# Optimization experiments

Hardware: AMD Instinct MI355X
Metric: run time of the kernel (lower is better)

## Reference

```python
import jax, jax.numpy as jnp
import numpy as np

D_MODEL = 1024
N_HEADS = 16
D_K = D_MODEL // N_HEADS
THETA = 10000.0


def _rope(x, token_positions):
    # x: [b, h, s, d_k]; interleaved RoPE (pairs at even/odd positions)
    half = D_K // 2
    inv_freq = 1.0 / (THETA ** (2.0 * jnp.arange(half, dtype=jnp.float32) / D_K))  # [half]
    angles = token_positions.astype(jnp.float32)[:, None] * inv_freq[None, :]      # [s, half]
    sin, cos = jnp.sin(angles), jnp.cos(angles)
    x_even = x[..., 0::2]
    x_odd = x[..., 1::2]
    out_even = cos * x_even - sin * x_odd
    out_odd = sin * x_even + cos * x_odd
    # interleave back: [..., half, 2] -> [..., d_k]
    return jnp.stack((out_even, out_odd), axis=-1).reshape(x.shape)


def setup_inputs() -> dict:
    key = jax.random.key(0)
    kx, kq, kk, kv, ko = jax.random.split(key, 5)
    b, s = 4, 2048
    std = (2.0 / (D_MODEL + D_MODEL)) ** 0.5
    return {
        "x": jax.random.normal(kx, (b, s, D_MODEL), dtype=jnp.float32),
        "Wq": jax.random.normal(kq, (D_MODEL, D_MODEL), dtype=jnp.float32) * std,
        "Wk": jax.random.normal(kk, (D_MODEL, D_MODEL), dtype=jnp.float32) * std,
        "Wv": jax.random.normal(kv, (D_MODEL, D_MODEL), dtype=jnp.float32) * std,
        "Wo": jax.random.normal(ko, (D_MODEL, D_MODEL), dtype=jnp.float32) * std,
        "token_positions": jnp.arange(s, dtype=jnp.int32),
    }


def reference(x, Wq, Wk, Wv, Wo, token_positions):
    b, s, _ = x.shape
    split = lambda t: t.reshape(b, s, N_HEADS, D_K).transpose(0, 2, 1, 3)  # b h s d
    q = split(x @ Wq.T)
    k = split(x @ Wk.T)
    v = split(x @ Wv.T)
    q = _rope(q, token_positions)
    k = _rope(k, token_positions)
    scores = jnp.einsum("bhnd,bhmd->bhnm", q, k) / jnp.sqrt(jnp.float32(D_K))
    causal = jnp.tril(jnp.ones((s, s), dtype=bool))
    scores = jnp.where(causal, scores, -jnp.inf)
    attn = jax.nn.softmax(scores, axis=-1)
    out = jnp.einsum("bhnm,bhmd->bhnd", attn, v)
    out = out.transpose(0, 2, 1, 3).reshape(b, s, D_MODEL)
    return out @ Wo.T
```

## Files before the change

kernel.cpp:

```cpp
#include <hip/hip_runtime.h>
#include <stdint.h>

typedef __attribute__((ext_vector_type(8))) __bf16 bf16x8;
typedef __attribute__((ext_vector_type(4))) float f32x4;
typedef __attribute__((ext_vector_type(16))) float f32x16;
typedef __attribute__((ext_vector_type(8))) unsigned short ushort8;

__device__ __forceinline__ unsigned short f2bf(float f){
  union { float f; unsigned int i; } v; v.f = f;
  unsigned int r = v.i + 0x7fffu + ((v.i >> 16) & 1u);
  return (unsigned short)(r >> 16);
}
__device__ __forceinline__ void gload16(const void* g, void* l){
  __builtin_amdgcn_global_load_lds((__attribute__((address_space(1))) void*)(g),
                                   (__attribute__((address_space(3))) void*)(l),
                                   16, 0, 0);
}
__device__ __forceinline__ unsigned int cvtpk(float lo, float hi){
  unsigned int r;
  asm("v_cvt_pk_bf16_f32 %0, %1, %2" : "=v"(r) : "v"(lo), "v"(hi));
  return r;
}
__device__ __forceinline__ float fexp2(float x){
  float r; asm("v_exp_f32 %0, %1" : "=v"(r) : "v"(x)); return r;
}
__device__ __forceinline__ bf16x8 ldsw(const char* tile, int row, int colb){
  return *(const bf16x8*)(tile + row*128 + (colb ^ ((row & 7) << 4)));
}

#define SEQ   2048
#define DM    1024
#define NH    16
#define DK    64
#define BATCH 4
#define MTOT  (BATCH*SEQ)
#define NX    (MTOT*DM)
#define NW    (DM*DM)

#define QSCALE 0.18033688011112f

__global__ __launch_bounds__(256) void k_tables(const int* __restrict__ pos,
                                                float* __restrict__ tab)
{
  const int idx = blockIdx.x * 256 + threadIdx.x;
  const int s = idx >> 5, i = idx & 31;
  const float inv = __expf(-0.28782313662425575f * (float)i);
  const float a = (float)pos[s] * inv;
  tab[2*idx]   = cosf(a);
  tab[2*idx+1] = sinf(a);
}

__global__ __launch_bounds__(256) void k_convert(
    const float* __restrict__ x,  const float* __restrict__ wq,
    const float* __restrict__ wk, const float* __restrict__ wv,
    const float* __restrict__ wo,
    unsigned short* __restrict__ xb, unsigned short* __restrict__ wb)
{
  const int tid = blockIdx.x * 256 + threadIdx.x;
  const long long e = (long long)tid * 8;
  const float* src; unsigned short* dst;
  if (e < NX) { src = x + e; dst = xb + e; }
  else {
    long long j = e - NX;
    int seg = (int)(j >> 20);
    long long off = j & 1048575;
    src = (seg==0?wq:seg==1?wk:seg==2?wv:wo) + off;
    dst = wb + (size_t)seg*NW + off;
  }
  const float4 a = *(const float4*)src;
  const float4 b = *(const float4*)(src + 4);
  uint4 o;
  o.x = (unsigned int)f2bf(a.x) | ((unsigned int)f2bf(a.y) << 16);
  o.y = (unsigned int)f2bf(a.z) | ((unsigned int)f2bf(a.w) << 16);
  o.z = (unsigned int)f2bf(b.x) | ((unsigned int)f2bf(b.y) << 16);
  o.w = (unsigned int)f2bf(b.z) | ((unsigned int)f2bf(b.w) << 16);
  *(uint4*)dst = o;
}

#define NT32 32
#define ABUF32  16384
#define BSTR32  24576

template<int MODE>
__global__ __launch_bounds__(512, 4) void k_gemm(
    const unsigned short* __restrict__ A,
    const unsigned short* __restrict__ Wb,
    unsigned short* __restrict__ D0,
    unsigned short* __restrict__ D1,
    unsigned short* __restrict__ D2,
    float* __restrict__ Dout,
    const float* __restrict__ tab)
{
  __shared__ __attribute__((aligned(16))) char lds_[3*BSTR32];
  const int tid  = threadIdx.x;
  const int lane = tid & 63;
  const int w    = tid >> 6;
  const int wm = w >> 1, wn = w & 1;

  const int bid = blockIdx.x;
  const int tq  = bid >> 3;
  const int m0  = ((bid & 7)*4 + (tq & 3)) * 256;
  const int r   = tq >> 2;
  const int n0  = (MODE == 0 ? (r & 7) : r) * 128;
  const int z   = (MODE == 0) ? (r >> 3) : 0;

  const unsigned short* W = Wb + (size_t)z * NW;
  unsigned short* Dh = (MODE == 0) ? ((z == 0) ? D0 : (z == 1) ? D1 : D2) : nullptr;
  const bool vtr = (MODE == 0) && (z == 2);

  f32x4 acc[4][4];
  #pragma unroll
  for (int i = 0; i < 4; ++i)
    #pragma unroll
    for (int j = 0; j < 4; ++j)
      acc[i][j] = (f32x4)0.0f;

  auto stA = [&](int buf, int t, int l){
    const int id = l*512 + tid;
    const int row = id >> 2, c = id & 3;
    gload16(A + (size_t)(m0 + row)*DM + t*32 + ((c ^ ((row >> 1) & 3)) << 3),
            lds_ + buf*BSTR32 + id*16);
  };
  auto stB = [&](int buf, int t){
    const int id = tid;
    const int row = id >> 2, c = id & 3;
    gload16(W + (size_t)(n0 + row)*DM + t*32 + ((c ^ ((row >> 1) & 3)) << 3),
            lds_ + buf*BSTR32 + ABUF32 + id*16);
  };
  auto ldA = [&](const char* Ab_, int i){
    const int row = wm*64 + i*16 + (lane & 15);
    const int c = (lane >> 4) ^ ((row >> 1) & 3);
    return *(const bf16x8*)(Ab_ + row*64 + (c << 4));
  };
  auto ldB = [&](const char* Bb_, int j){
    const int row = wn*64 + j*16 + (lane & 15);
    const int c = (lane >> 4) ^ ((row >> 1) & 3);
    return *(const bf16x8*)(Bb_ + row*64 + (c << 4));
  };

  stA(0, 0, 0); stA(0, 0, 1); stB(0, 0);
  stA(1, 1, 0); stA(1, 1, 1); stB(1, 1);
  asm volatile("s_waitcnt vmcnt(3)" ::: "memory");
  __builtin_amdgcn_s_barrier();

  int rb = 0, sb = 2;
  for (int t = 0; t < NT32; ++t){
    const char* Ab_ = lds_ + rb*BSTR32;
    const char* Bb_ = Ab_ + ABUF32;
    const bool st = (t + 2 < NT32);
    bf16x8 aF0, aF1, bF[4];

    aF0 = ldA(Ab_, 0); aF1 = ldA(Ab_, 1);
    bF[0] = ldB(Bb_, 0); bF[1] = ldB(Bb_, 1);
    bF[2] = ldB(Bb_, 2); bF[3] = ldB(Bb_, 3);
    if (st){ stA(sb, t+2, 0); stA(sb, t+2, 1); }
    __builtin_amdgcn_s_barrier();
    asm volatile("s_waitcnt lgkmcnt(0)" ::: "memory");
    __builtin_amdgcn_s_setprio(1);
    #pragma unroll
    for (int j = 0; j < 4; ++j){
      acc[0][j] = __builtin_amdgcn_mfma_f32_16x16x32_bf16(aF0, bF[j], acc[0][j], 0, 0, 0);
      acc[1][j] = __builtin_amdgcn_mfma_f32_16x16x32_bf16(aF1, bF[j], acc[1][j], 0, 0, 0);
    }
    __builtin_amdgcn_s_setprio(0);
    __builtin_amdgcn_s_barrier();

    aF0 = ldA(Ab_, 2); aF1 = ldA(Ab_, 3);
    if (st) stB(sb, t+2);
    __builtin_amdgcn_s_barrier();
    asm volatile("s_waitcnt lgkmcnt(0)" ::: "memory");
    __builtin_amdgcn_s_setprio(1);
    #pragma unroll
    for (int j = 0; j < 4; ++j){
      acc[2][j] = __builtin_amdgcn_mfma_f32_16x16x32_bf16(aF0, bF[j], acc[2][j], 0, 0, 0);
      acc[3][j] = __builtin_amdgcn_mfma_f32_16x16x32_bf16(aF1, bF[j], acc[3][j], 0, 0, 0);
    }
    __builtin_amdgcn_s_setprio(0);
    if (t < NT32-2)       asm volatile("s_waitcnt vmcnt(3)" ::: "memory");
    else if (t == NT32-2) asm volatile("s_waitcnt vmcnt(0)" ::: "memory");
    if (t < NT32-1) __builtin_amdgcn_s_barrier();

    rb = (rb == 2) ? 0 : rb + 1;
    sb = (sb == 2) ? 0 : sb + 1;
  }

  __syncthreads();
  float* T = (float*)lds_;
  #pragma unroll
  for (int h = 0; h < 2; ++h){
    if (h) __syncthreads();
    if ((wm >> 1) == h){
      #pragma unroll
      for (int i = 0; i < 4; ++i)
        #pragma unroll
        for (int j = 0; j < 4; ++j){
          const int n = wn*64 + j*16 + (lane & 15);
          #pragma unroll
          for (int rr = 0; rr < 4; ++rr){
            const int mh = (wm & 1)*64 + i*16 + ((lane >> 4) << 2) + rr;
            T[mh*128 + (n ^ ((mh & 7) << 2))] = acc[i][j][rr];
          }
        }
    }
    __syncthreads();
    if (MODE == 0 && vtr){
      const int nl = tid >> 2;
      const int sblk = tid & 3;
      const int d = nl & 63, hh = (n0 >> 6) + (nl >> 6);
      const int bidx = m0 >> 11;
      unsigned short* vrow = Dh + (((size_t)(bidx*NH + hh))*DK + d)*SEQ
                               + (m0 & 2047) + h*128;
      #pragma unroll
      for (int c = 0; c < 4; ++c){
        const int s0 = sblk*8 + c*32;
        float v[8];
        #pragma unroll
        for (int j2 = 0; j2 < 8; ++j2)
          v[j2] = T[(s0 + j2)*128 + (nl ^ (((s0 + j2) & 7) << 2))];
        uint4 ov;
        ov.x = cvtpk(v[0], v[1]); ov.y = cvtpk(v[2], v[3]);
        ov.z = cvtpk(v[4], v[5]); ov.w = cvtpk(v[6], v[7]);
        *(uint4*)(vrow + s0) = ov;
      }
    } else {
      const float scale = (MODE == 0 && z == 0) ? QSCALE : 1.0f;
      #pragma unroll
      for (int k = 0; k < 4; ++k){
        const int cid = k*512 + tid;
        const int d8   = cid & 7;
        const int sp_l = (cid >> 3) & 127;
        const int hc   = cid >> 10;
        const int nb   = hc*64 + d8*8;
        const int sw   = (sp_l & 7) << 2;
        const f32x4 c0 = *(const f32x4*)&T[sp_l*128 + (nb ^ sw)];
        const f32x4 c1 = *(const f32x4*)&T[sp_l*128 + ((nb + 4) ^ sw)];
        if (MODE == 1){
          float* dst = Dout + (size_t)(m0 + h*128 + sp_l)*DM + n0 + nb;
          *(f32x4*)dst = c0;
          *(f32x4*)(dst + 4) = c1;
        } else {
          const int mg = m0 + h*128 + sp_l;
          const int bidx = mg >> 11, sp = mg & 2047;
          const float4 t01 = *(const float4*)&tab[(size_t)sp*64 + d8*8];
          const float4 t23 = *(const float4*)&tab[(size_t)sp*64 + d8*8 + 4];
          const unsigned int u0 = cvtpk((t01.x*c0[0] - t01.y*c0[1])*scale,
                                        (t01.y*c0[0] + t01.x*c0[1])*scale);
          const unsigned int u1 = cvtpk((t01.z*c0[2] - t01.w*c0[3])*scale,
                                        (t01.w*c0[2] + t01.z*c0[3])*scale);
          const unsigned int u2 = cvtpk((t23.x*c1[0] - t23.y*c1[1])*scale,
                                        (t23.y*c1[0] + t23.x*c1[1])*scale);
          const unsigned int u3 = cvtpk((t23.z*c1[2] - t23.w*c1[3])*scale,
                                        (t23.w*c1[2] + t23.z*c1[3])*scale);
          const int hh = (n0 >> 6) + hc;
          uint4 ov; ov.x = u0; ov.y = u1; ov.z = u2; ov.w = u3;
          *(uint4*)(Dh + ((size_t)((bidx*NH + hh)*SEQ + sp))*DK + d8*8) = ov;
        }
      }
    }
  }
}

__global__ __launch_bounds__(512, 4) void k_attn(const unsigned short* __restrict__ Qh,
                                                 const unsigned short* __restrict__ Kh,
                                                 const unsigned short* __restrict__ Vt,
                                                 unsigned short* __restrict__ Ab)
{
  __shared__ uint4 ldsu[4096];
  char* base = (char*)ldsu;
  const int tid  = threadIdx.x;
  const int lane = tid & 63;
  const int w    = tid >> 6;
  const int ww   = w & 3;
  const int g    = w >> 2;
  const int tl   = tid & 255;
  const int l31  = lane & 31;
  const int hl   = lane >> 5;
  char* gb = base + g*32768;

  const int bh = blockIdx.x, jj = blockIdx.y;
  const unsigned short* Qb = Qh + (size_t)bh*(SEQ*DK);
  const unsigned short* Kb = Kh + (size_t)bh*(SEQ*DK);
  const unsigned short* Vb = Vt + (size_t)bh*(SEQ*DK);
  const int b = bh >> 4, hd = bh & 15;

  for (int pass = 0; pass < 2; ++pass){
    const int qt = pass ? jj : 15 - jj;
    const int q0 = qt * 128;
    const int qbase = q0 + ww*32;

    bf16x8 qf[4];
    #pragma unroll
    for (int t = 0; t < 4; ++t)
      qf[t] = *(const bf16x8*)(Qb + (size_t)(qbase + l31)*DK + t*16 + hl*8);

    f32x16 acc0 = (f32x16)0.0f, acc1 = (f32x16)0.0f;
    float lsum = 0.0f;

    const int nk = qt + 1;
    const int tbase = g * nk;
    const int wqmax = qbase + 31;

    auto stage = [&](int buf, int ktile){
      const int k0s = ktile * 64;
      char* Kd = gb + buf*16384;
      char* Vd = Kd + 8192;
      #pragma unroll
      for (int cc = 0; cc < 2; ++cc){
        const int f = cc*256 + tl;
        const int r = f >> 3, slot = f & 7;
        const int sw = ((slot ^ (r & 7)) << 3);
        gload16(Kb + (size_t)(k0s + r)*DK + sw, Kd + (cc*256 + ww*64)*16);
        gload16(Vb + (size_t)r*SEQ + k0s + sw, Vd + (cc*256 + ww*64)*16);
      }
    };

    if (pass) __syncthreads();
    stage(0, tbase);
    __syncthreads();
    int cur = 0;

    for (int kt = 0; kt < nk; ++kt){
      const int k0 = (tbase + kt) * 64;
      if (kt + 1 < nk) stage(cur ^ 1, tbase + kt + 1);
      if (k0 <= wqmax){
        const char* Ks = gb + cur*16384;
        const char* Vs = Ks + 8192;

        f32x16 sv0 = (f32x16)0.0f, sv1 = (f32x16)0.0f;
        __builtin_amdgcn_s_setprio(1);
        #pragma unroll
        for (int t = 0; t < 4; ++t){
          const int colb = t*32 + hl*16;
          const bf16x8 a0 = ldsw(Ks, l31, colb);
          const bf16x8 a1 = ldsw(Ks, 32 + l31, colb);
          sv0 = __builtin_amdgcn_mfma_f32_32x32x16_bf16(a0, qf[t], sv0, 0, 0, 0);
          sv1 = __builtin_amdgcn_mfma_f32_32x32x16_bf16(a1, qf[t], sv1, 0, 0, 0);
        }
        __builtin_amdgcn_s_setprio(0);

        if (k0 + 63 > qbase){
          const int q = qbase + l31;
          #pragma unroll
          for (int j = 0; j < 16; ++j){
            const int kv = k0 + (j&3) + 8*(j>>2) + 4*hl;
            if (kv > q)      sv0[j] = -1e30f;
            if (kv + 32 > q) sv1[j] = -1e30f;
          }
        }

        #pragma unroll
        for (int j = 0; j < 16; ++j){
          sv0[j] = fexp2(sv0[j]);
          sv1[j] = fexp2(sv1[j]);
        }
        float ts[8];
        #pragma unroll
        for (int j = 0; j < 8; ++j)
          ts[j] = (sv0[j] + sv0[j+8]) + (sv1[j] + sv1[j+8]);
        #pragma unroll
        for (int off = 4; off; off >>= 1)
          #pragma unroll
          for (int j = 0; j < off; ++j)
            ts[j] += ts[j+off];
        lsum += ts[0] + __shfl_xor(ts[0], 32, 64);

        __builtin_amdgcn_s_setprio(1);
        #pragma unroll
        for (int t = 0; t < 4; ++t){
          f32x16& s = (t < 2) ? sv0 : sv1;
          const int b0v = (t & 1) * 8;
          const unsigned int A0 = cvtpk(s[b0v+0], s[b0v+1]);
          const unsigned int A1 = cvtpk(s[b0v+2], s[b0v+3]);
          const unsigned int B0 = cvtpk(s[b0v+4], s[b0v+5]);
          const unsigned int B1 = cvtpk(s[b0v+6], s[b0v+7]);
          const unsigned int s0 = hl ? A0 : B0;
          const unsigned int s1 = hl ? A1 : B1;
          const unsigned int r0 = (unsigned int)__shfl_xor((int)s0, 32, 64);
          const unsigned int r1 = (unsigned int)__shfl_xor((int)s1, 32, 64);
          union { unsigned int u[4]; bf16x8 v; } f;
          f.u[0] = hl ? r0 : A0; f.u[1] = hl ? r1 : A1;
          f.u[2] = hl ? B0 : r0; f.u[3] = hl ? B1 : r1;
          const int colb = t*32 + hl*16;
          const bf16x8 v0 = ldsw(Vs, l31, colb);
          const bf16x8 v1 = ldsw(Vs, 32 + l31, colb);
          acc0 = __builtin_amdgcn_mfma_f32_32x32x16_bf16(v0, f.v, acc0, 0, 0, 0);
          acc1 = __builtin_amdgcn_mfma_f32_32x32x16_bf16(v1, f.v, acc1, 0, 0, 0);
        }
        __builtin_amdgcn_s_setprio(0);
      }
      __syncthreads();
      cur ^= 1;
    }

    if (g == 1){
      char* cw = base + ww*9216 + lane*144;
      #pragma unroll
      for (int q4 = 0; q4 < 4; ++q4){
        *(f32x4*)(cw + q4*16)      = (f32x4){acc0[4*q4], acc0[4*q4+1], acc0[4*q4+2], acc0[4*q4+3]};
        *(f32x4*)(cw + 64 + q4*16) = (f32x4){acc1[4*q4], acc1[4*q4+1], acc1[4*q4+2], acc1[4*q4+3]};
      }
      *(float*)(cw + 128) = lsum;
    }
    __syncthreads();
    if (g == 0){
      const char* cr = base + ww*9216 + lane*144;
      const float l1 = *(const float*)(cr + 128);
      const float linv = 1.0f / (lsum + l1);
      unsigned short* orow = Ab + ((size_t)(b*SEQ + qbase + l31))*DM + hd*DK;
      #pragma unroll
      for (int mt = 0; mt < 2; ++mt){
        #pragma unroll
        for (int g4 = 0; g4 < 4; ++g4){
          const f32x16& a = mt ? acc1 : acc0;
          const f32x4 o = *(const f32x4*)(cr + mt*64 + g4*16);
          const unsigned int u0 = cvtpk((a[4*g4+0] + o[0])*linv, (a[4*g4+1] + o[1])*linv);
          const unsigned int u1 = cvtpk((a[4*g4+2] + o[2])*linv, (a[4*g4+3] + o[3])*linv);
          *(unsigned long long*)(orow + mt*32 + g4*8 + hl*4) =
              (unsigned long long)u0 | ((unsigned long long)u1 << 32);
        }
      }
    }
  }
}

extern "C" void kernel_launch(void* const* d_in, const int* in_sizes, int n_in,
                              void* d_out, int out_size, void* d_ws, size_t ws_size,
                              hipStream_t stream)
{
  (void)in_sizes; (void)n_in; (void)out_size;
  const float* x  = (const float*)d_in[0];
  const float* wq = (const float*)d_in[1];
  const float* wk = (const float*)d_in[2];
  const float* wv = (const float*)d_in[3];
  const float* wo = (const float*)d_in[4];
  const int* pos  = (const int*)d_in[5];
  float* out = (float*)d_out;

  if (ws_size < 92800000u) return;
  char* ws = (char*)d_ws;
  unsigned short* xb = (unsigned short*)(ws);
  unsigned short* wb = (unsigned short*)(ws + 16777216);
  unsigned short* Qh = (unsigned short*)(ws + 25165824);
  unsigned short* Kh = (unsigned short*)(ws + 41943040);
  unsigned short* Vt = (unsigned short*)(ws + 75497472);
  float* tab         = (float*)(ws + 92274688);

  k_tables  <<<256, 256, 0, stream>>>(pos, tab);
  k_convert <<<6144, 256, 0, stream>>>(x, wq, wk, wv, wo, xb, wb);
  k_gemm<0> <<<768, 512, 0, stream>>>(xb, wb, Qh, Kh, Vt, nullptr, tab);
  k_attn    <<<dim3(64, 8), 512, 0, stream>>>(Qh, Kh, Vt, xb);
  k_gemm<1> <<<256, 512, 0, stream>>>(xb, wb + 3*NW, nullptr, nullptr,
                                      nullptr, out, nullptr);
}
```

Baseline: 160.4 us.

## Drop intra-iteration GEMM barriers and fold RoPE table build into convert kernel

The GEMM main loop now reads all four A fragments and four B fragments up front and issues all async global-to-LDS stores for tile t+2 at once. It then runs the full 4x4 MFMA block, removing two barriers and an explicit lgkmcnt wait per k-step. The triple buffering plus the end-of-iteration barrier is relied on to keep the overwritten buffer safe. Separately, the RoPE cos/sin table computation is merged into the bf16 conversion kernel as extra blocks, saving one kernel launch. Holding more fragments live raises register pressure, and MFMA work no longer interleaves with the LDS reads of the second half.

```diff
diff --git a/kernel.cpp b/kernel.cpp
--- a/kernel.cpp
+++ b/kernel.cpp
@@ -39,42 +39,41 @@
 
 #define QSCALE 0.18033688011112f
 
-__global__ __launch_bounds__(256) void k_tables(const int* __restrict__ pos,
-                                                float* __restrict__ tab)
-{
-  const int idx = blockIdx.x * 256 + threadIdx.x;
-  const int s = idx >> 5, i = idx & 31;
-  const float inv = __expf(-0.28782313662425575f * (float)i);
-  const float a = (float)pos[s] * inv;
-  tab[2*idx]   = cosf(a);
-  tab[2*idx+1] = sinf(a);
-}
-
 __global__ __launch_bounds__(256) void k_convert(
     const float* __restrict__ x,  const float* __restrict__ wq,
     const float* __restrict__ wk, const float* __restrict__ wv,
     const float* __restrict__ wo,
-    unsigned short* __restrict__ xb, unsigned short* __restrict__ wb)
+    unsigned short* __restrict__ xb, unsigned short* __restrict__ wb,
+    const int* __restrict__ pos, float* __restrict__ tab)
 {
   const int tid = blockIdx.x * 256 + threadIdx.x;
-  const long long e = (long long)tid * 8;
-  const float* src; unsigned short* dst;
-  if (e < NX) { src = x + e; dst = xb + e; }
-  else {
-    long long j = e - NX;
-    int seg = (int)(j >> 20);
-    long long off = j & 1048575;
-    src = (seg==0?wq:seg==1?wk:seg==2?wv:wo) + off;
-    dst = wb + (size_t)seg*NW + off;
+  if (tid < 1572864){
+    const long long e = (long long)tid * 8;
+    const float* src; unsigned short* dst;
+    if (e < NX) { src = x + e; dst = xb + e; }
+    else {
+      long long j = e - NX;
+      int seg = (int)(j >> 20);
+      long long off = j & 1048575;
+      src = (seg==0?wq:seg==1?wk:seg==2?wv:wo) + off;
+      dst = wb + (size_t)seg*NW + off;
+    }
+    const float4 a = *(const float4*)src;
+    const float4 b = *(const float4*)(src + 4);
+    uint4 o;
+    o.x = (unsigned int)f2bf(a.x) | ((unsigned int)f2bf(a.y) << 16);
+    o.y = (unsigned int)f2bf(a.z) | ((unsigned int)f2bf(a.w) << 16);
+    o.z = (unsigned int)f2bf(b.x) | ((unsigned int)f2bf(b.y) << 16);
+    o.w = (unsigned int)f2bf(b.z) | ((unsigned int)f2bf(b.w) << 16);
+    *(uint4*)dst = o;
+  } else {
+    const int idx = tid - 1572864;
+    const int s = idx >> 5, i = idx & 31;
+    const float inv = __expf(-0.28782313662425575f * (float)i);
+    const float a = (float)pos[s] * inv;
+    tab[2*idx]   = cosf(a);
+    tab[2*idx+1] = sinf(a);
   }
-  const float4 a = *(const float4*)src;
-  const float4 b = *(const float4*)(src + 4);
-  uint4 o;
-  o.x = (unsigned int)f2bf(a.x) | ((unsigned int)f2bf(a.y) << 16);
-  o.y = (unsigned int)f2bf(a.z) | ((unsigned int)f2bf(a.w) << 16);
-  o.z = (unsigned int)f2bf(b.x) | ((unsigned int)f2bf(b.y) << 16);
-  o.w = (unsigned int)f2bf(b.z) | ((unsigned int)f2bf(b.w) << 16);
-  *(uint4*)dst = o;
 }
 
 #define NT32 32
@@ -148,33 +147,19 @@
     const char* Ab_ = lds_ + rb*BSTR32;
     const char* Bb_ = Ab_ + ABUF32;
     const bool st = (t + 2 < NT32);
-    bf16x8 aF0, aF1, bF[4];
-
-    aF0 = ldA(Ab_, 0); aF1 = ldA(Ab_, 1);
+    bf16x8 aF[4], bF[4];
+
+    aF[0] = ldA(Ab_, 0); aF[1] = ldA(Ab_, 1);
+    aF[2] = ldA(Ab_, 2); aF[3] = ldA(Ab_, 3);
     bF[0] = ldB(Bb_, 0); bF[1] = ldB(Bb_, 1);
     bF[2] = ldB(Bb_, 2); bF[3] = ldB(Bb_, 3);
-    if (st){ stA(sb, t+2, 0); stA(sb, t+2, 1); }
-    __builtin_amdgcn_s_barrier();
-    asm volatile("s_waitcnt lgkmcnt(0)" ::: "memory");
+    if (st){ stA(sb, t+2, 0); stA(sb, t+2, 1); stB(sb, t+2); }
     __builtin_amdgcn_s_setprio(1);
     #pragma unroll
-    for (int j = 0; j < 4; ++j){
-      acc[0][j] = __builtin_amdgcn_mfma_f32_16x16x32_bf16(aF0, bF[j], acc[0][j], 0, 0, 0);
-      acc[1][j] = __builtin_amdgcn_mfma_f32_16x16x32_bf16(aF1, bF[j], acc[1][j], 0, 0, 0);
-    }
-    __builtin_amdgcn_s_setprio(0);
-    __builtin_amdgcn_s_barrier();
-
-    aF0 = ldA(Ab_, 2); aF1 = ldA(Ab_, 3);
-    if (st) stB(sb, t+2);
-    __builtin_amdgcn_s_barrier();
-    asm volatile("s_waitcnt lgkmcnt(0)" ::: "memory");
-    __builtin_amdgcn_s_setprio(1);
-    #pragma unroll
-    for (int j = 0; j < 4; ++j){
-      acc[2][j] = __builtin_amdgcn_mfma_f32_16x16x32_bf16(aF0, bF[j], acc[2][j], 0, 0, 0);
-      acc[3][j] = __builtin_amdgcn_mfma_f32_16x16x32_bf16(aF1, bF[j], acc[3][j], 0, 0, 0);
-    }
+    for (int i = 0; i < 4; ++i)
+      #pragma unroll
+      for (int j = 0; j < 4; ++j)
+        acc[i][j] = __builtin_amdgcn_mfma_f32_16x16x32_bf16(aF[i], bF[j], acc[i][j], 0, 0, 0);
     __builtin_amdgcn_s_setprio(0);
     if (t < NT32-2)       asm volatile("s_waitcnt vmcnt(3)" ::: "memory");
     else if (t == NT32-2) asm volatile("s_waitcnt vmcnt(0)" ::: "memory");
@@ -445,8 +430,7 @@
   unsigned short* Vt = (unsigned short*)(ws + 75497472);
   float* tab         = (float*)(ws + 92274688);
 
-  k_tables  <<<256, 256, 0, stream>>>(pos, tab);
-  k_convert <<<6144, 256, 0, stream>>>(x, wq, wk, wv, wo, xb, wb);
+  k_convert <<<6400, 256, 0, stream>>>(x, wq, wk, wv, wo, xb, wb, pos, tab);
   k_gemm<0> <<<768, 512, 0, stream>>>(xb, wb, Qh, Kh, Vt, nullptr, tab);
   k_attn    <<<dim3(64, 8), 512, 0, stream>>>(Qh, Kh, Vt, xb);
   k_gemm<1> <<<256, 512, 0, stream>>>(xb, wb + 3*NW, nullptr, nullptr,
```

Result: faster. 153.4 us (median of 2 runs) (-4.4%).
